# Optimization experiments

Measured on AMD Instinct MI355X. Metric: run time of the kernel, lower is better.

The kernel has to match this reference:

```python
import jax, jax.numpy as jnp
import numpy as np

B, LT, D, N, H = 16, 512, 1024, 4096, 16
LN_EPS = 1e-5


def setup_inputs() -> dict:
    key = jax.random.key(0)
    ks = jax.random.split(key, 10)
    s = 0.02
    struct_token = jax.random.normal(ks[0], (N, D), dtype=jnp.float32)
    text_token = jax.random.normal(ks[1], (B, LT, D), dtype=jnp.float32)
    # contiguous, sorted segment ids: 256 struct tokens per batch element
    struct_batch = jnp.repeat(jnp.arange(B, dtype=jnp.int32), N // B)
    return {
        "struct_token": struct_token,
        "text_token": text_token,
        "in_proj_w": jax.random.normal(ks[2], (3 * D, D), dtype=jnp.float32) * s,
        "in_proj_b": jnp.zeros((3 * D,), jnp.float32),
        "attn_out_w": jax.random.normal(ks[3], (D, D), dtype=jnp.float32) * s,
        "attn_out_b": jnp.zeros((D,), jnp.float32),
        "ln_g": jnp.ones((D,), jnp.float32),
        "ln_b": jnp.zeros((D,), jnp.float32),
        "proj_w": jax.random.normal(ks[4], (D, D), dtype=jnp.float32) * s,
        "proj_b": jnp.zeros((D,), jnp.float32),
        "struct_batch": struct_batch,
        "L_max": N // B,
    }


def reference(struct_token, text_token, in_proj_w, in_proj_b, attn_out_w,
              attn_out_b, ln_g, ln_b, proj_w, proj_b, struct_batch, L_max):
    Bq = text_token.shape[0]
    Dm = struct_token.shape[-1]
    dh = Dm // H
    Ntok = struct_token.shape[0]

    # ---- ragged pad-pack (struct_batch is sorted/contiguous per segment) ----
    counts = jnp.bincount(struct_batch, length=Bq)                 # [B]
    starts = jnp.concatenate([jnp.zeros((1,), counts.dtype),
                              jnp.cumsum(counts)[:-1]])            # [B]
    pos = jnp.arange(Ntok) - starts[struct_batch]                  # [N] position in segment
    padded = jnp.zeros((Bq, L_max, Dm), struct_token.dtype)
    padded = padded.at[struct_batch, pos].set(struct_token)        # [B, Ls, D]

    # ---- nn.MultiheadAttention (batch_first): Q=padded, K=V=text ----
    wq, wk, wv = in_proj_w[:Dm], in_proj_w[Dm:2 * Dm], in_proj_w[2 * Dm:]
    bq, bk, bv = in_proj_b[:Dm], in_proj_b[Dm:2 * Dm], in_proj_b[2 * Dm:]
    q = (padded @ wq.T + bq).reshape(Bq, L_max, H, dh)
    k = (text_token @ wk.T + bk).reshape(Bq, -1, H, dh)
    v = (text_token @ wv.T + bv).reshape(Bq, -1, H, dh)
    scores = jnp.einsum('bqhd,bkhd->bhqk', q, k) / jnp.sqrt(jnp.float32(dh))
    attn = jax.nn.softmax(scores, axis=-1)
    ctx = jnp.einsum('bhqk,bkhd->bqhd', attn, v).reshape(Bq, L_max, Dm)
    fused = ctx @ attn_out_w.T + attn_out_b                        # [B, Ls, D]

    # ---- LayerNorm + output projection ----
    mu = fused.mean(-1, keepdims=True)
    var = fused.var(-1, keepdims=True)
    fused = (fused - mu) * jax.lax.rsqrt(var + LN_EPS) * ln_g + ln_b
    fused = fused @ proj_w.T + proj_b

    # ---- unpack valid tokens + scatter-mean over segments ----
    tok = fused[struct_batch, pos]                                 # [N, D]
    seg_sum = jax.ops.segment_sum(tok, struct_batch, num_segments=Bq)
    return seg_sum / jnp.maximum(counts, 1)[:, None].astype(seg_sum.dtype)
```

## Files before the change

### kernel.cpp

```cpp
#include <hip/hip_runtime.h>

constexpr int B  = 16;
constexpr int LT = 512;
constexpr int D  = 1024;
constexpr int N  = 4096;
constexpr int H  = 16;
constexpr int DH = D / H;
constexpr int LMAX = N / B;
constexpr float LN_EPS = 1e-5f;

typedef short  s16x8 __attribute__((ext_vector_type(8)));
typedef float  f32x4 __attribute__((ext_vector_type(4)));

__device__ __forceinline__ unsigned short f2bf(float x) {
    unsigned int u = __float_as_uint(x);
    unsigned int r = (u + 0x7fffu + ((u >> 16) & 1u)) >> 16;
    return (unsigned short)r;
}
__device__ __forceinline__ float bf2f(unsigned short u) {
    return __uint_as_float((unsigned int)u << 16);
}

__device__ __forceinline__ void load_lds16(const void* g, void* l) {
    __builtin_amdgcn_global_load_lds(
        (const __attribute__((address_space(1))) unsigned int*)g,
        (__attribute__((address_space(3))) unsigned int*)l, 16, 0, 0);
}

__global__ __launch_bounds__(256) void cast3_prep(
        const float* __restrict__ x0, unsigned short* __restrict__ y0, int n0,
        const float* __restrict__ x1, unsigned short* __restrict__ y1, int n1,
        const float* __restrict__ x2, unsigned short* __restrict__ y2, int n2,
        const int* __restrict__ sb, int* __restrict__ counts, int* __restrict__ starts) {
    __shared__ int s_counts[B];
    int t = threadIdx.x;
    if (blockIdx.x == 6144) {
        if (t < B) s_counts[t] = 0;
        __syncthreads();
        for (int i = t; i < N; i += 256) atomicAdd(&s_counts[sb[i]], 1);
        __syncthreads();
        if (t == 0) {
            int run = 0;
            for (int b = 0; b < B; b++) { starts[b] = run; run += s_counts[b]; }
        }
        if (t < B) counts[t] = s_counts[t];
        return;
    }
    long long i = (long long)(blockIdx.x * 256 + t) * 8;
    const float* x; unsigned short* y;
    if (i < n0)                { x = x0 + i; y = y0 + i; }
    else if (i < (long long)n0 + n1) { long long j = i - n0; x = x1 + j; y = y1 + j; }
    else if (i < (long long)n0 + n1 + n2) { long long j = i - n0 - n1; x = x2 + j; y = y2 + j; }
    else return;
    float4 a = *(const float4*)x;
    float4 b = *(const float4*)(x + 4);
    ushort4 o1, o2;
    o1.x = f2bf(a.x); o1.y = f2bf(a.y); o1.z = f2bf(a.z); o1.w = f2bf(a.w);
    o2.x = f2bf(b.x); o2.y = f2bf(b.y); o2.z = f2bf(b.z); o2.w = f2bf(b.w);
    *(ushort4*)y = o1;
    *(ushort4*)(y + 4) = o2;
}

__global__ void scatter_full(const float* __restrict__ st,
                             const int* __restrict__ counts,
                             const int* __restrict__ starts,
                             unsigned short* __restrict__ padded) {
    int p = blockIdx.x, b = blockIdx.y;
    int d = threadIdx.x * 4;
    size_t off = ((size_t)(b * LMAX + p)) * D + d;
    ushort4 o = {0, 0, 0, 0};
    if (p < counts[b]) {
        float4 v = *(const float4*)&st[(size_t)(starts[b] + p) * D + d];
        o.x = f2bf(v.x); o.y = f2bf(v.y); o.z = f2bf(v.z); o.w = f2bf(v.w);
    }
    *(ushort4*)&padded[off] = o;
}

constexpr int PANEL = 128 * 32;

template<typename Epi>
__device__ __forceinline__ void gemm_tile_e(const unsigned short* __restrict__ A,
                                            const unsigned short* __restrict__ W,
                                            int K, int kbeg, int kend, int m0, int n0,
                                            unsigned short* As, unsigned short* Bs,
                                            Epi&& epi) {
    const int tid  = threadIdx.x;
    const int lane = tid & 63;
    const int wave = tid >> 6;
    const int wm = (wave >> 1) * 64, wn = (wave & 1) * 64;

    const int srow = tid >> 2;
    const int scol = (tid & 3) * 8;
    const unsigned short* Ag = A + (size_t)(m0 + srow) * K + scol;
    const unsigned short* Wg = W + (size_t)(n0 + srow) * K + scol;
    unsigned short* Asl = As + tid * 8;
    unsigned short* Bsl = Bs + tid * 8;

    const int fm = lane & 15;
    const int fk = (lane >> 4) * 8;

    f32x4 acc[4][4];
#pragma unroll
    for (int i = 0; i < 4; i++)
#pragma unroll
        for (int j = 0; j < 4; j++) acc[i][j] = (f32x4){0.f, 0.f, 0.f, 0.f};

    for (int k0 = kbeg; k0 < kend; k0 += 64) {
        __syncthreads();
        load_lds16(Ag + k0, Asl);
        load_lds16(Ag + (size_t)64 * K + k0, Asl + 64 * 32);
        load_lds16(Wg + k0, Bsl);
        load_lds16(Wg + (size_t)64 * K + k0, Bsl + 64 * 32);
        load_lds16(Ag + k0 + 32, Asl + PANEL);
        load_lds16(Ag + (size_t)64 * K + k0 + 32, Asl + PANEL + 64 * 32);
        load_lds16(Wg + k0 + 32, Bsl + PANEL);
        load_lds16(Wg + (size_t)64 * K + k0 + 32, Bsl + PANEL + 64 * 32);
        __syncthreads();

#pragma unroll
        for (int hp = 0; hp < 2; hp++) {
            const unsigned short* Ap = As + hp * PANEL;
            const unsigned short* Bp = Bs + hp * PANEL;
            s16x8 af[4], bf[4];
#pragma unroll
            for (int i = 0; i < 4; i++) {
                af[i] = *(const s16x8*)&Ap[(wm + i * 16 + fm) * 32 + fk];
                bf[i] = *(const s16x8*)&Bp[(wn + i * 16 + fm) * 32 + fk];
            }
#pragma unroll
            for (int i = 0; i < 4; i++)
#pragma unroll
                for (int j = 0; j < 4; j++)
                    acc[i][j] = __builtin_amdgcn_mfma_f32_16x16x32_bf16(af[i], bf[j], acc[i][j], 0, 0, 0);
        }
    }

    const int fr = (lane >> 4) * 4;
#pragma unroll
    for (int j = 0; j < 4; j++) {
        int col = n0 + wn + j * 16 + fm;
#pragma unroll
        for (int i = 0; i < 4; i++) {
            int row = m0 + wm + i * 16 + fr;
#pragma unroll
            for (int r = 0; r < 4; r++)
                epi(row + r, col, acc[i][j][r]);
        }
    }
}

__global__ __launch_bounds__(256) void qkv_fused(const unsigned short* __restrict__ padded,
                                                 const unsigned short* __restrict__ text,
                                                 const unsigned short* __restrict__ wqkv,
                                                 const float* __restrict__ bqkv,
                                                 unsigned short* __restrict__ qpack,
                                                 unsigned short* __restrict__ kpack,
                                                 unsigned short* __restrict__ vpack) {
    __shared__ __align__(16) unsigned short As[2 * PANEL];
    __shared__ __align__(16) unsigned short Bs[2 * PANEL];
    int flat = blockIdx.x;
    if (flat < 256) {
        int m = flat & 31, n = flat >> 5;
        gemm_tile_e(padded, wqkv, D, 0, D, m * 128, n * 128, As, Bs,
            [&](int mm, int col, float v) {
                float val = v + bqkv[col];
                int b = mm >> 8, q = mm & 255;
                int h = col >> 6, d = col & 63;
                qpack[(size_t)(b * H + h) * 16384 + (d >> 3) * 2048 + q * 8 + (d & 7)] = f2bf(val);
            });
    } else if (flat < 768) {
        int f = flat - 256;
        int m = f & 63, n = f >> 6;
        gemm_tile_e(text, wqkv + (size_t)D * D, D, 0, D, m * 128, n * 128, As, Bs,
            [&](int mm, int col, float v) {
                float val = v + bqkv[D + col];
                int b = mm >> 9, key = mm & 511;
                int h = col >> 6, d = col & 63;
                kpack[(size_t)(b * H + h) * 32768 + (d >> 3) * 4096 + key * 8 + (d & 7)] = f2bf(val);
            });
    } else {
        int f = flat - 768;
        int m = f >> 6, n = f & 63;
        gemm_tile_e(wqkv + 2 * (size_t)D * D, text, D, 0, D, m * 128, n * 128, As, Bs,
            [&](int mm, int col, float v) {
                float val = v + bqkv[2 * D + mm];
                int h = mm >> 6, d = mm & 63;
                int b = col >> 9, key = col & 511;
                vpack[(size_t)(b * H + h) * 32768 + (key >> 3) * 512 + d * 8 + (key & 7)] = f2bf(val);
            });
    }
}

__global__ __launch_bounds__(256) void gemm_bf2(const unsigned short* __restrict__ A,
                                                const unsigned short* __restrict__ W,
                                                unsigned short* __restrict__ C0,
                                                unsigned short* __restrict__ C1,
                                                int Nn, int K) {
    __shared__ __align__(16) unsigned short As[2 * PANEL];
    __shared__ __align__(16) unsigned short Bs[2 * PANEL];
    int id = blockIdx.x;
    int kh = id >> 8;
    int n  = (id & 255) >> 5;
    int m  = id & 31;
    unsigned short* C = kh ? C1 : C0;
    gemm_tile_e(A, W, K, kh * 512, (kh + 1) * 512, m * 128, n * 128, As, Bs,
        [&](int mm, int col, float v) {
            C[(size_t)mm * Nn + col] = f2bf(v);
        });
}

constexpr int PKW = 72;

__global__ __launch_bounds__(512) void attn_mfma(const unsigned short* __restrict__ qpack,
                                                 const unsigned short* __restrict__ kpack,
                                                 const unsigned short* __restrict__ vpack,
                                                 unsigned short* __restrict__ ctx) {
    __shared__ __align__(16) unsigned short KV[16384];
    __shared__ __align__(16) unsigned short Ps[8 * 16 * PKW];

    const int tid = threadIdx.x;
    const int lane = tid & 63;
    const int wv = tid >> 6;
    const int fm = lane & 15;
    const int quad = lane >> 4;
    const int h = blockIdx.x, b = blockIdx.y, half = blockIdx.z;
    const int q0 = half * 128 + wv * 16;

    const unsigned short* qp = qpack + (size_t)(b * H + h) * 16384;
    const unsigned short* kp = kpack + (size_t)(b * H + h) * 32768;
    const unsigned short* vp = vpack + (size_t)(b * H + h) * 32768;

    const s16x8 aq0 = *(const s16x8*)&qp[quad * 2048 + (q0 + fm) * 8];
    const s16x8 aq1 = *(const s16x8*)&qp[(4 + quad) * 2048 + (q0 + fm) * 8];

    f32x4 sc[32];

    for (int kc = 0; kc < 2; kc++) {
        __syncthreads();
#pragma unroll
        for (int it = 0; it < 4; it++) {
            int f = it * 512 + tid;
            load_lds16(kp + (f >> 8) * 4096 + kc * 2048 + (f & 255) * 8, KV + f * 8);
        }
        __syncthreads();
#pragma unroll
        for (int t = 0; t < 16; t++) {
            s16x8 bk0 = *(const s16x8*)&KV[quad * 2048 + (t * 16 + fm) * 8];
            s16x8 bk1 = *(const s16x8*)&KV[(4 + quad) * 2048 + (t * 16 + fm) * 8];
            f32x4 a = (f32x4){0.f, 0.f, 0.f, 0.f};
            a = __builtin_amdgcn_mfma_f32_16x16x32_bf16(aq0, bk0, a, 0, 0, 0);
            a = __builtin_amdgcn_mfma_f32_16x16x32_bf16(aq1, bk1, a, 0, 0, 0);
            sc[kc * 16 + t] = a;
        }
    }

    const float scale = 0.125f;
    float mx[4], l[4], inv[4];
#pragma unroll
    for (int r = 0; r < 4; r++) {
        float m = sc[0][r];
#pragma unroll
        for (int t = 1; t < 32; t++) m = fmaxf(m, sc[t][r]);
        mx[r] = m;
    }
#pragma unroll
    for (int o = 1; o < 16; o <<= 1)
#pragma unroll
        for (int r = 0; r < 4; r++) mx[r] = fmaxf(mx[r], __shfl_xor(mx[r], o));
#pragma unroll
    for (int r = 0; r < 4; r++) l[r] = 0.f;
#pragma unroll
    for (int t = 0; t < 32; t++)
#pragma unroll
        for (int r = 0; r < 4; r++) {
            float e = __expf((sc[t][r] - mx[r]) * scale);
            sc[t][r] = e;
            l[r] += e;
        }
#pragma unroll
    for (int o = 1; o < 16; o <<= 1)
#pragma unroll
        for (int r = 0; r < 4; r++) l[r] += __shfl_xor(l[r], o);
#pragma unroll
    for (int r = 0; r < 4; r++) inv[r] = 1.f / l[r];

    f32x4 co[4];
#pragma unroll
    for (int n = 0; n < 4; n++) co[n] = (f32x4){0.f, 0.f, 0.f, 0.f};
    unsigned short* Pw = Ps + wv * (16 * PKW);

    for (int vc = 0; vc < 2; vc++) {
        __syncthreads();
#pragma unroll
        for (int it = 0; it < 4; it++) {
            int f = it * 512 + tid;
            load_lds16(vp + vc * 16384 + f * 8, KV + f * 8);
        }
        __syncthreads();
        for (int cs = 0; cs < 4; cs++) {
            int c = vc * 4 + cs;
#pragma unroll
            for (int tt = 0; tt < 4; tt++)
#pragma unroll
                for (int r = 0; r < 4; r++)
                    Pw[(quad * 4 + r) * PKW + tt * 16 + fm] = f2bf(sc[c * 4 + tt][r]);
#pragma unroll
            for (int s = 0; s < 2; s++) {
                s16x8 ap = *(const s16x8*)&Pw[fm * PKW + s * 32 + quad * 8];
#pragma unroll
                for (int n = 0; n < 4; n++) {
                    s16x8 bv = *(const s16x8*)&KV[(cs * 8 + s * 4 + quad) * 512 + (n * 16 + fm) * 8];
                    co[n] = __builtin_amdgcn_mfma_f32_16x16x32_bf16(ap, bv, co[n], 0, 0, 0);
                }
            }
        }
    }

    const size_t obase = (size_t)(b * LMAX + q0) * D + h * DH;
#pragma unroll
    for (int n = 0; n < 4; n++)
#pragma unroll
        for (int r = 0; r < 4; r++)
            ctx[obase + (size_t)(quad * 4 + r) * D + n * 16 + fm] = f2bf(co[n][r] * inv[r]);
}

__global__ __launch_bounds__(256) void lnmean_kernel(const unsigned short* __restrict__ f1a,
                                                     const unsigned short* __restrict__ f1b,
                                                     const float* __restrict__ bo,
                                                     const float* __restrict__ g,
                                                     const float* __restrict__ bb,
                                                     const int* __restrict__ counts,
                                                     float* __restrict__ msum) {
    int b = blockIdx.x;
    int t = threadIdx.x;
    int wv = t >> 6, lane = t & 63;
    int cnt = counts[b];
    int s0 = blockIdx.y * 32 + wv * 8;
    int s1 = min(cnt, s0 + 8);

    float4 gg[4], bv[4], bo4[4];
#pragma unroll
    for (int c = 0; c < 4; c++) {
        gg[c]  = *(const float4*)&g[c * 256 + lane * 4];
        bv[c]  = *(const float4*)&bb[c * 256 + lane * 4];
        bo4[c] = *(const float4*)&bo[c * 256 + lane * 4];
    }
    float4 acc[4];
#pragma unroll
    for (int c = 0; c < 4; c++) acc[c] = (float4){0.f, 0.f, 0.f, 0.f};

    for (int s = s0; s < s1; s++) {
        size_t rbase = ((size_t)(b * LMAX + s)) * D;
        float4 v[4];
        float sm = 0.f, ss = 0.f;
#pragma unroll
        for (int c = 0; c < 4; c++) {
            ushort4 ua = *(const ushort4*)&f1a[rbase + c * 256 + lane * 4];
            ushort4 ub = *(const ushort4*)&f1b[rbase + c * 256 + lane * 4];
            v[c].x = bf2f(ua.x) + bf2f(ub.x) + bo4[c].x;
            v[c].y = bf2f(ua.y) + bf2f(ub.y) + bo4[c].y;
            v[c].z = bf2f(ua.z) + bf2f(ub.z) + bo4[c].z;
            v[c].w = bf2f(ua.w) + bf2f(ub.w) + bo4[c].w;
            sm += v[c].x + v[c].y + v[c].z + v[c].w;
            ss += v[c].x * v[c].x + v[c].y * v[c].y + v[c].z * v[c].z + v[c].w * v[c].w;
        }
#pragma unroll
        for (int o = 32; o; o >>= 1) { sm += __shfl_xor(sm, o); ss += __shfl_xor(ss, o); }
        float mu = sm * (1.f / D);
        float var = ss * (1.f / D) - mu * mu;
        float r = rsqrtf(var + LN_EPS);
#pragma unroll
        for (int c = 0; c < 4; c++) {
            acc[c].x += (v[c].x - mu) * r * gg[c].x + bv[c].x;
            acc[c].y += (v[c].y - mu) * r * gg[c].y + bv[c].y;
            acc[c].z += (v[c].z - mu) * r * gg[c].z + bv[c].z;
            acc[c].w += (v[c].w - mu) * r * gg[c].w + bv[c].w;
        }
    }
    float inv = 1.f / (float)max(cnt, 1);
#pragma unroll
    for (int c = 0; c < 4; c++) {
        int base = b * D + c * 256 + lane * 4;
        atomicAdd(&msum[base + 0], acc[c].x * inv);
        atomicAdd(&msum[base + 1], acc[c].y * inv);
        atomicAdd(&msum[base + 2], acc[c].z * inv);
        atomicAdd(&msum[base + 3], acc[c].w * inv);
    }
}

__global__ __launch_bounds__(256) void tproj_kernel(const float* __restrict__ msum,
                                                    const float* __restrict__ W,
                                                    const float* __restrict__ bias,
                                                    float* __restrict__ out) {
    int lane = threadIdx.x & 63;
    int n = blockIdx.x * 4 + (threadIdx.x >> 6);
    float4 wr[4];
#pragma unroll
    for (int i = 0; i < 4; i++)
        wr[i] = *(const float4*)&W[(size_t)n * D + i * 256 + lane * 4];
    float bn = bias[n];
    for (int b = 0; b < B; b++) {
        float s = 0.f;
#pragma unroll
        for (int i = 0; i < 4; i++) {
            float4 m4 = *(const float4*)&msum[(size_t)b * D + i * 256 + lane * 4];
            s += m4.x * wr[i].x + m4.y * wr[i].y + m4.z * wr[i].z + m4.w * wr[i].w;
        }
#pragma unroll
        for (int o = 32; o; o >>= 1) s += __shfl_xor(s, o);
        if (lane == 0) out[(size_t)b * D + n] = s + bn;
    }
}

extern "C" void kernel_launch(void* const* d_in, const int* in_sizes, int n_in,
                              void* d_out, int out_size, void* d_ws, size_t ws_size,
                              hipStream_t stream) {
    const float* struct_token = (const float*)d_in[0];
    const float* text_token   = (const float*)d_in[1];
    const float* in_proj_w    = (const float*)d_in[2];
    const float* in_proj_b    = (const float*)d_in[3];
    const float* attn_out_w   = (const float*)d_in[4];
    const float* attn_out_b   = (const float*)d_in[5];
    const float* ln_g         = (const float*)d_in[6];
    const float* ln_b         = (const float*)d_in[7];
    const float* proj_w       = (const float*)d_in[8];
    const float* proj_b       = (const float*)d_in[9];
    const int*   sb           = (const int*)d_in[10];
    float* out = (float*)d_out;

    const size_t MQ  = (size_t)B * LMAX;
    const size_t MKV = (size_t)B * LT;

    char* p = (char*)d_ws;
    unsigned short* padded_b = (unsigned short*)p;  p += MQ * D * 2;
    unsigned short* text_b   = (unsigned short*)p;  p += MKV * D * 2;
    unsigned short* wqkv_b   = (unsigned short*)p;  p += (size_t)3 * D * D * 2;
    unsigned short* wattn_b  = (unsigned short*)p;  p += (size_t)D * D * 2;
    unsigned short* qpack    = (unsigned short*)p;  p += MQ * D * 2;
    unsigned short* kpack    = (unsigned short*)p;  p += MKV * D * 2;
    unsigned short* vpack    = (unsigned short*)p;  p += MKV * D * 2;
    unsigned short* ctx_b    = (unsigned short*)p;  p += MQ * D * 2;
    unsigned short* f1a      = (unsigned short*)p;  p += MQ * D * 2;
    unsigned short* f1b      = (unsigned short*)p;  p += MQ * D * 2;
    float* msum = (float*)p;  p += (size_t)B * D * 4;
    int* counts = (int*)p;  p += B * 4;
    int* starts = (int*)p;  p += B * 4;

    hipMemsetAsync(msum, 0, (size_t)B * D * 4, stream);

    cast3_prep<<<6145, 256, 0, stream>>>(
        text_token, text_b, (int)(MKV * D),
        in_proj_w,  wqkv_b, 3 * D * D,
        attn_out_w, wattn_b, D * D,
        sb, counts, starts);

    scatter_full<<<dim3(LMAX, B), 256, 0, stream>>>(struct_token, counts, starts, padded_b);

    qkv_fused<<<1280, 256, 0, stream>>>(padded_b, text_b, wqkv_b, in_proj_b,
                                        qpack, kpack, vpack);

    attn_mfma<<<dim3(H, B, 2), 512, 0, stream>>>(qpack, kpack, vpack, ctx_b);

    gemm_bf2<<<512, 256, 0, stream>>>(ctx_b, wattn_b, f1a, f1b, D, D);

    lnmean_kernel<<<dim3(B, 8), 256, 0, stream>>>(f1a, f1b, attn_out_b, ln_g, ln_b, counts, msum);

    tproj_kernel<<<256, 256, 0, stream>>>(msum, proj_w, proj_b, out);
}
```

Baseline: 257.2 us.

## Rewrite bf16 GEMM core as 256x128 triple-buffered pipelined tile with swizzled LDS

```diff
diff --git a/kernel.cpp b/kernel.cpp
--- a/kernel.cpp
+++ b/kernel.cpp
@@ -76,102 +76,155 @@
     *(ushort4*)&padded[off] = o;
 }
 
-constexpr int PANEL = 128 * 32;
-
 template<typename Epi>
-__device__ __forceinline__ void gemm_tile_e(const unsigned short* __restrict__ A,
+__device__ __forceinline__ void gemm256x128(const unsigned short* __restrict__ A,
                                             const unsigned short* __restrict__ W,
                                             int K, int kbeg, int kend, int m0, int n0,
-                                            unsigned short* As, unsigned short* Bs,
+                                            unsigned short* __restrict__ As,
+                                            unsigned short* __restrict__ Bs,
                                             Epi&& epi) {
     const int tid  = threadIdx.x;
     const int lane = tid & 63;
-    const int wave = tid >> 6;
-    const int wm = (wave >> 1) * 64, wn = (wave & 1) * 64;
-
-    const int srow = tid >> 2;
-    const int scol = (tid & 3) * 8;
-    const unsigned short* Ag = A + (size_t)(m0 + srow) * K + scol;
-    const unsigned short* Wg = W + (size_t)(n0 + srow) * K + scol;
-    unsigned short* Asl = As + tid * 8;
-    unsigned short* Bsl = Bs + tid * 8;
-
-    const int fm = lane & 15;
-    const int fk = (lane >> 4) * 8;
-
-    f32x4 acc[4][4];
-#pragma unroll
-    for (int i = 0; i < 4; i++)
-#pragma unroll
-        for (int j = 0; j < 4; j++) acc[i][j] = (f32x4){0.f, 0.f, 0.f, 0.f};
-
-    for (int k0 = kbeg; k0 < kend; k0 += 64) {
-        __syncthreads();
-        load_lds16(Ag + k0, Asl);
-        load_lds16(Ag + (size_t)64 * K + k0, Asl + 64 * 32);
-        load_lds16(Wg + k0, Bsl);
-        load_lds16(Wg + (size_t)64 * K + k0, Bsl + 64 * 32);
-        load_lds16(Ag + k0 + 32, Asl + PANEL);
-        load_lds16(Ag + (size_t)64 * K + k0 + 32, Asl + PANEL + 64 * 32);
-        load_lds16(Wg + k0 + 32, Bsl + PANEL);
-        load_lds16(Wg + (size_t)64 * K + k0 + 32, Bsl + PANEL + 64 * 32);
-        __syncthreads();
-
-#pragma unroll
-        for (int hp = 0; hp < 2; hp++) {
-            const unsigned short* Ap = As + hp * PANEL;
-            const unsigned short* Bp = Bs + hp * PANEL;
-            s16x8 af[4], bf[4];
-#pragma unroll
-            for (int i = 0; i < 4; i++) {
-                af[i] = *(const s16x8*)&Ap[(wm + i * 16 + fm) * 32 + fk];
-                bf[i] = *(const s16x8*)&Bp[(wn + i * 16 + fm) * 32 + fk];
+    const int wid  = tid >> 6;
+    const int wr   = wid >> 2;
+    const int wc   = wid & 3;
+    const int fm   = lane & 15;
+    const int quad = lane >> 4;
+
+    const int NK = (kend - kbeg) >> 6;
+
+    f32x4 acc[8][2];
+#pragma unroll
+    for (int i = 0; i < 8; i++)
+#pragma unroll
+        for (int j = 0; j < 2; j++) acc[i][j] = (f32x4){0.f, 0.f, 0.f, 0.f};
+
+    auto stage = [&](int s) {
+        const int k0  = kbeg + (s << 6);
+        const int buf = s - (s / 3) * 3;
+        unsigned short* Ad = As + buf * 16384;
+        unsigned short* Bd = Bs + buf * 8192;
+#pragma unroll
+        for (int r = 0; r < 4; r++) {
+            int ci  = r * 512 + tid;
+            int row = ci >> 3;
+            int sg  = (ci & 7) ^ (row & 7);
+            load_lds16(A + (size_t)(m0 + row) * K + k0 + sg * 8, Ad + ci * 8);
+        }
+#pragma unroll
+        for (int r = 0; r < 2; r++) {
+            int ci  = r * 512 + tid;
+            int row = ci >> 3;
+            int sg  = (ci & 7) ^ (row & 7);
+            load_lds16(W + (size_t)(n0 + row) * K + k0 + sg * 8, Bd + ci * 8);
+        }
+    };
+
+    stage(0);
+    stage(1);
+
+    for (int s = 0; s < NK; s++) {
+        if (s + 1 < NK) asm volatile("s_waitcnt vmcnt(6)" ::: "memory");
+        else            asm volatile("s_waitcnt vmcnt(0)" ::: "memory");
+        __builtin_amdgcn_s_barrier();
+        __builtin_amdgcn_sched_barrier(0);
+
+        if (s + 2 < NK) stage(s + 2);
+
+        const int buf = s - (s / 3) * 3;
+        const unsigned short* Ab = As + buf * 16384;
+        const unsigned short* Bb = Bs + buf * 8192;
+
+        s16x8 bfr[2][2];
+#pragma unroll
+        for (int j = 0; j < 2; j++) {
+            int row = wc * 32 + j * 16 + fm;
+#pragma unroll
+            for (int kk = 0; kk < 2; kk++) {
+                int sl = (kk * 4 + quad) ^ (row & 7);
+                bfr[j][kk] = *(const s16x8*)&Bb[row * 64 + sl * 8];
             }
+        }
+
+        s16x8 afr[4][2];
+#pragma unroll
+        for (int i = 0; i < 4; i++) {
+            int row = wr * 128 + i * 16 + fm;
+#pragma unroll
+            for (int kk = 0; kk < 2; kk++) {
+                int sl = (kk * 4 + quad) ^ (row & 7);
+                afr[i][kk] = *(const s16x8*)&Ab[row * 64 + sl * 8];
+            }
+        }
+        __builtin_amdgcn_s_setprio(1);
+#pragma unroll
+        for (int kk = 0; kk < 2; kk++)
 #pragma unroll
             for (int i = 0; i < 4; i++)
 #pragma unroll
-                for (int j = 0; j < 4; j++)
-                    acc[i][j] = __builtin_amdgcn_mfma_f32_16x16x32_bf16(af[i], bf[j], acc[i][j], 0, 0, 0);
-        }
-    }
-
-    const int fr = (lane >> 4) * 4;
-#pragma unroll
-    for (int j = 0; j < 4; j++) {
-        int col = n0 + wn + j * 16 + fm;
+                for (int j = 0; j < 2; j++)
+                    acc[i][j] = __builtin_amdgcn_mfma_f32_16x16x32_bf16(afr[i][kk], bfr[j][kk], acc[i][j], 0, 0, 0);
+        __builtin_amdgcn_s_setprio(0);
+
 #pragma unroll
         for (int i = 0; i < 4; i++) {
-            int row = m0 + wm + i * 16 + fr;
-#pragma unroll
-            for (int r = 0; r < 4; r++)
-                epi(row + r, col, acc[i][j][r]);
-        }
-    }
-}
-
-__global__ __launch_bounds__(256) void qkv_fused(const unsigned short* __restrict__ padded,
-                                                 const unsigned short* __restrict__ text,
-                                                 const unsigned short* __restrict__ wqkv,
-                                                 const float* __restrict__ bqkv,
-                                                 unsigned short* __restrict__ qpack,
-                                                 unsigned short* __restrict__ kpack,
-                                                 unsigned short* __restrict__ vpack) {
-    __shared__ __align__(16) unsigned short As[2 * PANEL];
-    __shared__ __align__(16) unsigned short Bs[2 * PANEL];
-    int flat = blockIdx.x;
-    if (flat < 256) {
-        int m = flat & 31, n = flat >> 5;
-        gemm_tile_e(padded, wqkv, D, 0, D, m * 128, n * 128, As, Bs,
+            int row = wr * 128 + 64 + i * 16 + fm;
+#pragma unroll
+            for (int kk = 0; kk < 2; kk++) {
+                int sl = (kk * 4 + quad) ^ (row & 7);
+                afr[i][kk] = *(const s16x8*)&Ab[row * 64 + sl * 8];
+            }
+        }
+        __builtin_amdgcn_s_setprio(1);
+#pragma unroll
+        for (int kk = 0; kk < 2; kk++)
+#pragma unroll
+            for (int i = 0; i < 4; i++)
+#pragma unroll
+                for (int j = 0; j < 2; j++)
+                    acc[4 + i][j] = __builtin_amdgcn_mfma_f32_16x16x32_bf16(afr[i][kk], bfr[j][kk], acc[4 + i][j], 0, 0, 0);
+        __builtin_amdgcn_s_setprio(0);
+    }
+
+    const int fr = quad * 4;
+#pragma unroll
+    for (int h = 0; h < 2; h++)
+#pragma unroll
+        for (int i = 0; i < 4; i++)
+#pragma unroll
+            for (int j = 0; j < 2; j++) {
+                int row = m0 + wr * 128 + h * 64 + i * 16 + fr;
+                int col = n0 + wc * 32 + j * 16 + fm;
+#pragma unroll
+                for (int r = 0; r < 4; r++)
+                    epi(row + r, col, acc[h * 4 + i][j][r]);
+            }
+}
+
+__global__ __launch_bounds__(512, 2) void qkv_fused(const unsigned short* __restrict__ padded,
+                                                    const unsigned short* __restrict__ text,
+                                                    const unsigned short* __restrict__ wqkv,
+                                                    const float* __restrict__ bqkv,
+                                                    unsigned short* __restrict__ qpack,
+                                                    unsigned short* __restrict__ kpack,
+                                                    unsigned short* __restrict__ vpack) {
+    __shared__ __align__(16) unsigned short As[3 * 16384];
+    __shared__ __align__(16) unsigned short Bs[3 * 8192];
+    int orig = blockIdx.x;
+    int id = (orig & 7) * 80 + (orig >> 3);
+    if (id < 128) {
+        int mt = id >> 3, nt = id & 7;
+        gemm256x128(padded, wqkv, D, 0, D, mt * 256, nt * 128, As, Bs,
             [&](int mm, int col, float v) {
                 float val = v + bqkv[col];
                 int b = mm >> 8, q = mm & 255;
                 int h = col >> 6, d = col & 63;
                 qpack[(size_t)(b * H + h) * 16384 + (d >> 3) * 2048 + q * 8 + (d & 7)] = f2bf(val);
             });
-    } else if (flat < 768) {
-        int f = flat - 256;
-        int m = f & 63, n = f >> 6;
-        gemm_tile_e(text, wqkv + (size_t)D * D, D, 0, D, m * 128, n * 128, As, Bs,
+    } else if (id < 384) {
+        int f = id - 128;
+        int mt = f >> 3, nt = f & 7;
+        gemm256x128(text, wqkv + (size_t)D * D, D, 0, D, mt * 256, nt * 128, As, Bs,
             [&](int mm, int col, float v) {
                 float val = v + bqkv[D + col];
                 int b = mm >> 9, key = mm & 511;
@@ -179,9 +232,9 @@
                 kpack[(size_t)(b * H + h) * 32768 + (d >> 3) * 4096 + key * 8 + (d & 7)] = f2bf(val);
             });
     } else {
-        int f = flat - 768;
-        int m = f >> 6, n = f & 63;
-        gemm_tile_e(wqkv + 2 * (size_t)D * D, text, D, 0, D, m * 128, n * 128, As, Bs,
+        int f = id - 384;
+        int mt = f >> 6, nt = f & 63;
+        gemm256x128(wqkv + 2 * (size_t)D * D, text, D, 0, D, mt * 256, nt * 128, As, Bs,
             [&](int mm, int col, float v) {
                 float val = v + bqkv[2 * D + mm];
                 int h = mm >> 6, d = mm & 63;
@@ -191,19 +244,20 @@
     }
 }
 
-__global__ __launch_bounds__(256) void gemm_bf2(const unsigned short* __restrict__ A,
-                                                const unsigned short* __restrict__ W,
-                                                unsigned short* __restrict__ C0,
-                                                unsigned short* __restrict__ C1,
-                                                int Nn, int K) {
-    __shared__ __align__(16) unsigned short As[2 * PANEL];
-    __shared__ __align__(16) unsigned short Bs[2 * PANEL];
-    int id = blockIdx.x;
-    int kh = id >> 8;
-    int n  = (id & 255) >> 5;
-    int m  = id & 31;
+__global__ __launch_bounds__(512, 2) void gemm_bf2(const unsigned short* __restrict__ A,
+                                                   const unsigned short* __restrict__ W,
+                                                   unsigned short* __restrict__ C0,
+                                                   unsigned short* __restrict__ C1,
+                                                   int Nn, int K) {
+    __shared__ __align__(16) unsigned short As[3 * 16384];
+    __shared__ __align__(16) unsigned short Bs[3 * 8192];
+    int orig = blockIdx.x;
+    int id = (orig & 7) * 32 + (orig >> 3);
+    int kh = id >> 7;
+    int f  = id & 127;
+    int mt = f >> 3, nt = f & 7;
     unsigned short* C = kh ? C1 : C0;
-    gemm_tile_e(A, W, K, kh * 512, (kh + 1) * 512, m * 128, n * 128, As, Bs,
+    gemm256x128(A, W, K, kh * 512, (kh + 1) * 512, mt * 256, nt * 128, As, Bs,
         [&](int mm, int col, float v) {
             C[(size_t)mm * Nn + col] = f2bf(v);
         });
@@ -456,12 +510,12 @@
 
     scatter_full<<<dim3(LMAX, B), 256, 0, stream>>>(struct_token, counts, starts, padded_b);
 
-    qkv_fused<<<1280, 256, 0, stream>>>(padded_b, text_b, wqkv_b, in_proj_b,
-                                        qpack, kpack, vpack);
+    qkv_fused<<<640, 512, 0, stream>>>(padded_b, text_b, wqkv_b, in_proj_b,
+                                       qpack, kpack, vpack);
 
     attn_mfma<<<dim3(H, B, 2), 512, 0, stream>>>(qpack, kpack, vpack, ctx_b);
 
-    gemm_bf2<<<512, 256, 0, stream>>>(ctx_b, wattn_b, f1a, f1b, D, D);
+    gemm_bf2<<<256, 512, 0, stream>>>(ctx_b, wattn_b, f1a, f1b, D, D);
 
     lnmean_kernel<<<dim3(B, 8), 256, 0, stream>>>(f1a, f1b, attn_out_b, ln_g, ln_b, counts, msum);
 
```

Measured after the change: 265.1 us. 1.03x slower.
